# Optimization experiments

Measured on AMD Instinct MI355X. Metric: run time of the kernel, lower is better.

Reference implementation:

```python
import jax, jax.numpy as jnp
import numpy as np

ALPHA = 0.2  # leaky_relu negative slope
NEG = -1e20


def gat_conv(x, edges, W, a, b):
    # x: [B,N,F], W: [F,O], a: [2O,1], b: [O]
    h = jnp.einsum('bnf,fo->bno', x, W)
    O = W.shape[1]
    # cat([h[src], h[tgt]]) @ a  ==  h[src]@a[:O] + h[tgt]@a[O:]
    s1 = h @ a[:O, 0]   # [B,N]
    s2 = h @ a[O:, 0]   # [B,N]
    src, tgt = edges[0], edges[1]
    e = jax.nn.leaky_relu(s1[:, src] + s2[:, tgt], ALPHA)  # [B,E]
    B, N, _ = h.shape
    # dense NxN scatter-assign, as in the original module
    att = jnp.full((B, N, N), NEG, dtype=h.dtype).at[:, src, tgt].set(e)
    att = jax.nn.softmax(att, axis=-1)
    return jnp.einsum('bnm,bmo->bno', att, h) + b


def setup_inputs() -> dict:
    key = jax.random.key(0)
    ks = jax.random.split(key, 8)
    B, N, E = 2, 2048, 32768
    Fin, nhid, nhead, Fout = 256, 8, 8, 64
    x = jax.random.normal(ks[0], (B, N, Fin), dtype=jnp.float32)
    edges = jax.random.randint(ks[1], (2, E), 0, N)
    # xavier-like init (gain 1.414)
    W_h = jax.random.normal(ks[2], (nhead, Fin, nhid), dtype=jnp.float32) * (1.414 / np.sqrt(Fin))
    a_h = jax.random.normal(ks[3], (nhead, 2 * nhid, 1), dtype=jnp.float32) * 0.3
    b_h = jnp.zeros((nhead, nhid), dtype=jnp.float32)
    W_o = jax.random.normal(ks[4], (nhid * nhead, Fout), dtype=jnp.float32) * (1.414 / np.sqrt(nhid * nhead))
    a_o = jax.random.normal(ks[5], (2 * Fout, 1), dtype=jnp.float32) * 0.1
    b_o = jnp.zeros((Fout,), dtype=jnp.float32)
    return {'x': x, 'edges': edges, 'W_h': W_h, 'a_h': a_h, 'b_h': b_h,
            'W_o': W_o, 'a_o': a_o, 'b_o': b_o}


def reference(x, edges, W_h, a_h, b_h, W_o, a_o, b_o):
    B, N, _ = x.shape
    # nhead parallel GATConv heads, concatenated along feature dim
    heads = jax.vmap(lambda W, a, b: gat_conv(x, edges, W, a, b))(W_h, a_h, b_h)  # [H,B,N,nhid]
    x1 = jax.nn.elu(jnp.moveaxis(heads, 0, 2).reshape(B, N, -1))  # [B,N,H*nhid]
    out = gat_conv(x1, edges, W_o, a_o, b_o)  # single out head (mean of 1)
    return jax.nn.log_softmax(out, axis=1)  # softmax over the node dim, per original
```

## Files before the change

kernel.cpp:

```cpp
#include <hip/hip_runtime.h>

#define BB   2
#define NN   2048
#define FIN  256
#define HH   8
#define NHID 8
#define C1   64
#define FOUT 64
#define MAXD 192
#define FASTD 64
#define GB1  512

__global__ __launch_bounds__(256)
void k_front(const float* __restrict__ x, const float* __restrict__ Wh,
             const float* __restrict__ ah, const int* __restrict__ edges, int E,
             float* __restrict__ h1, float* __restrict__ s1h, float* __restrict__ s2h,
             int* __restrict__ cnt, int* __restrict__ csr)
{
    __shared__ float xs[8][FIN];
    int tid = threadIdx.x;

    if (blockIdx.x >= GB1) {
        int e = (blockIdx.x - GB1) * 256 + tid;
        if (e < E) {
            int s = edges[e], t = edges[E + e];
            int pos = atomicAdd(&cnt[s], 1);
            if (pos < MAXD) csr[s * MAXD + pos] = t;
        }
        return;
    }

    int base = blockIdx.x * 8;
    const float4* xv = (const float4*)(x + (size_t)base * FIN);
    float4* xsv = (float4*)&xs[0][0];
    xsv[tid] = xv[tid];
    xsv[tid + 256] = xv[tid + 256];
    __syncthreads();

    int wave = tid >> 6, lane = tid & 63;
    int head = lane >> 3, k = lane & 7;
    const float* Wp = Wh + head * FIN * NHID + k;
    int n0 = wave * 2;
    const float4* xr0 = (const float4*)xs[n0 + 0];
    const float4* xr1 = (const float4*)xs[n0 + 1];
    float a0 = 0.f, a1 = 0.f;
#pragma unroll 8
    for (int ff = 0; ff < FIN / 4; ++ff) {
        float4 v0 = xr0[ff], v1 = xr1[ff];
        float w0 = Wp[(4 * ff + 0) * NHID];
        float w1 = Wp[(4 * ff + 1) * NHID];
        float w2 = Wp[(4 * ff + 2) * NHID];
        float w3 = Wp[(4 * ff + 3) * NHID];
        a0 += w0 * v0.x; a0 += w1 * v0.y; a0 += w2 * v0.z; a0 += w3 * v0.w;
        a1 += w0 * v1.x; a1 += w1 * v1.y; a1 += w2 * v1.z; a1 += w3 * v1.w;
    }
    size_t hb = (size_t)(base + n0) * C1 + lane;
    h1[hb] = a0; h1[hb + C1] = a1;

    float c1 = ah[head * 16 + k], c2 = ah[head * 16 + 8 + k];
    float p0 = a0 * c1, p1 = a1 * c1;
    float q0 = a0 * c2, q1 = a1 * c2;
    for (int o = 1; o < 8; o <<= 1) {
        p0 += __shfl_xor(p0, o); p1 += __shfl_xor(p1, o);
        q0 += __shfl_xor(q0, o); q1 += __shfl_xor(q1, o);
    }
    if (k == 0) {
        float ps[2] = {p0, p1}, qs[2] = {q0, q1};
#pragma unroll
        for (int j = 0; j < 2; ++j) {
            int bn = base + n0 + j;
            s1h[(size_t)bn * HH + head] = ps[j];
            s2h[(size_t)bn * HH + head] = qs[j];
        }
    }
}

__global__ __launch_bounds__(256)
void k_att1g2(const float* __restrict__ h1, const float* __restrict__ s1h,
              const float* __restrict__ s2h, const float* __restrict__ bh,
              const int* __restrict__ cnt, int* __restrict__ csr,
              const float* __restrict__ Wo, const float* __restrict__ ao,
              float* __restrict__ h2, float* __restrict__ s1o, float* __restrict__ s2o)
{
    __shared__ int tg4[4][MAXD];
    __shared__ float es4[4][FASTD][HH];
    __shared__ float xs4[4][C1];
    int tid = threadIdx.x, w = tid >> 6, lane = tid & 63;
    int* tg = tg4[w];
    float* xs = xs4[w];
    int bn = blockIdx.x * 4 + w;
    int b = bn >> 11, n = bn & (NN - 1);
    int head = lane >> 3;

    int d = cnt[n]; if (d > MAXD) d = MAXD;
    for (int l = lane; l < d; l += 64) tg[l] = csr[n * MAXD + l];
    for (int l = lane; l < d; l += 64) {
        int t = tg[l], f = 0;
        for (int j = 0; j < l; ++j) f |= (tg[j] == t);
        if (f) tg[l] = -1;
    }
    for (int l = lane; l < d; l += 64) csr[n * MAXD + l] = tg[l];

    const float* hp = h1 + (size_t)b * NN * C1 + lane;
    float out;
    if (d == 0) {
        float acc = 0.f;
        for (int j = 0; j < NN; ++j) acc += hp[(size_t)j * C1];
        out = acc * (1.0f / NN);
    } else if (d <= FASTD) {
        const float* s2b = s2h + (size_t)b * NN * HH;
        for (int idx = lane; idx < d * HH; idx += 64) {
            int l = idx >> 3, hh = idx & 7;
            int t = tg[l];
            es4[w][l][hh] = s2b[(size_t)(t < 0 ? 0 : t) * HH + hh];
        }
        float s1 = s1h[(size_t)bn * HH + head];
        float m = -3.4e38f;
        for (int p = 0; p < d; ++p) {
            float ee = s1 + es4[w][p][head];
            ee = ee > 0.f ? ee : 0.2f * ee;
            m = fmaxf(m, tg[p] < 0 ? -3.4e38f : ee);
        }
        float den = 0.f, acc = 0.f;
        int p = 0;
        for (; p + 4 <= d; p += 4) {
            int t0 = tg[p], t1 = tg[p + 1], t2 = tg[p + 2], t3 = tg[p + 3];
            float v0 = hp[(size_t)(t0 < 0 ? 0 : t0) * C1];
            float v1 = hp[(size_t)(t1 < 0 ? 0 : t1) * C1];
            float v2 = hp[(size_t)(t2 < 0 ? 0 : t2) * C1];
            float v3 = hp[(size_t)(t3 < 0 ? 0 : t3) * C1];
            float e0 = s1 + es4[w][p + 0][head]; e0 = e0 > 0.f ? e0 : 0.2f * e0;
            float e1 = s1 + es4[w][p + 1][head]; e1 = e1 > 0.f ? e1 : 0.2f * e1;
            float e2 = s1 + es4[w][p + 2][head]; e2 = e2 > 0.f ? e2 : 0.2f * e2;
            float e3 = s1 + es4[w][p + 3][head]; e3 = e3 > 0.f ? e3 : 0.2f * e3;
            float w0 = t0 < 0 ? 0.f : expf(e0 - m);
            float w1 = t1 < 0 ? 0.f : expf(e1 - m);
            float w2 = t2 < 0 ? 0.f : expf(e2 - m);
            float w3 = t3 < 0 ? 0.f : expf(e3 - m);
            den += w0; acc += w0 * v0;
            den += w1; acc += w1 * v1;
            den += w2; acc += w2 * v2;
            den += w3; acc += w3 * v3;
        }
        for (; p < d; ++p) {
            int t = tg[p];
            float v = hp[(size_t)(t < 0 ? 0 : t) * C1];
            float ee = s1 + es4[w][p][head];
            ee = ee > 0.f ? ee : 0.2f * ee;
            float wt = t < 0 ? 0.f : expf(ee - m);
            den += wt; acc += wt * v;
        }
        out = acc / den;
    } else {
        float s1 = s1h[(size_t)bn * HH + head];
        const float* s2b = s2h + (size_t)b * NN * HH;
        float m = -3.4e38f;
        for (int p = 0; p < d; ++p) {
            int t = tg[p]; if (t < 0) continue;
            float ee = s1 + s2b[(size_t)t * HH + head];
            ee = ee > 0.f ? ee : 0.2f * ee;
            m = fmaxf(m, ee);
        }
        float den = 0.f, acc = 0.f;
        for (int p = 0; p < d; ++p) {
            int t = tg[p]; if (t < 0) continue;
            float ee = s1 + s2b[(size_t)t * HH + head];
            ee = ee > 0.f ? ee : 0.2f * ee;
            float wt = expf(ee - m);
            den += wt;
            acc += wt * hp[(size_t)t * C1];
        }
        out = acc / den;
    }
    out += bh[lane];
    xs[lane] = out > 0.f ? out : (expf(out) - 1.f);

    float acc2 = 0.f;
#pragma unroll 16
    for (int f = 0; f < C1; ++f) acc2 += xs[f] * Wo[f * FOUT + lane];
    h2[(size_t)bn * FOUT + lane] = acc2;
    float p = acc2 * ao[lane];
    float q = acc2 * ao[FOUT + lane];
    for (int o = 1; o < 64; o <<= 1) { p += __shfl_xor(p, o); q += __shfl_xor(q, o); }
    if (lane == 0) { s1o[bn] = p; s2o[bn] = q; }
}

__global__ __launch_bounds__(256)
void k_att2(const float* __restrict__ h2, const float* __restrict__ s1o,
            const float* __restrict__ s2o, const float* __restrict__ bo,
            const int* __restrict__ cnt, const int* __restrict__ csr,
            float* __restrict__ out2T)
{
    __shared__ int tg4[4][MAXD];
    __shared__ float es4[4][FASTD];
    int tid = threadIdx.x, w = tid >> 6, lane = tid & 63;
    int* tg = tg4[w];
    int bn = blockIdx.x * 4 + w;
    int b = bn >> 11, n = bn & (NN - 1);

    int d = cnt[n]; if (d > MAXD) d = MAXD;
    for (int l = lane; l < d; l += 64) tg[l] = csr[n * MAXD + l];

    const float* hp = h2 + (size_t)b * NN * FOUT + lane;
    const float* s2p = s2o + b * NN;
    float out;
    if (d == 0) {
        float acc = 0.f;
        for (int j = 0; j < NN; ++j) acc += hp[(size_t)j * FOUT];
        out = acc * (1.0f / NN);
    } else if (d <= FASTD) {
        for (int l = lane; l < d; l += 64) {
            int t = tg[l];
            es4[w][l] = s2p[t < 0 ? 0 : t];
        }
        float s1 = s1o[bn];
        float m = -3.4e38f;
        for (int p = 0; p < d; ++p) {
            float ee = s1 + es4[w][p];
            ee = ee > 0.f ? ee : 0.2f * ee;
            m = fmaxf(m, tg[p] < 0 ? -3.4e38f : ee);
        }
        float den = 0.f, acc = 0.f;
        int p = 0;
        for (; p + 4 <= d; p += 4) {
            int t0 = tg[p], t1 = tg[p + 1], t2 = tg[p + 2], t3 = tg[p + 3];
            float v0 = hp[(size_t)(t0 < 0 ? 0 : t0) * FOUT];
            float v1 = hp[(size_t)(t1 < 0 ? 0 : t1) * FOUT];
            float v2 = hp[(size_t)(t2 < 0 ? 0 : t2) * FOUT];
            float v3 = hp[(size_t)(t3 < 0 ? 0 : t3) * FOUT];
            float e0 = s1 + es4[w][p + 0]; e0 = e0 > 0.f ? e0 : 0.2f * e0;
            float e1 = s1 + es4[w][p + 1]; e1 = e1 > 0.f ? e1 : 0.2f * e1;
            float e2 = s1 + es4[w][p + 2]; e2 = e2 > 0.f ? e2 : 0.2f * e2;
            float e3 = s1 + es4[w][p + 3]; e3 = e3 > 0.f ? e3 : 0.2f * e3;
            float w0 = t0 < 0 ? 0.f : expf(e0 - m);
            float w1 = t1 < 0 ? 0.f : expf(e1 - m);
            float w2 = t2 < 0 ? 0.f : expf(e2 - m);
            float w3 = t3 < 0 ? 0.f : expf(e3 - m);
            den += w0; acc += w0 * v0;
            den += w1; acc += w1 * v1;
            den += w2; acc += w2 * v2;
            den += w3; acc += w3 * v3;
        }
        for (; p < d; ++p) {
            int t = tg[p];
            float v = hp[(size_t)(t < 0 ? 0 : t) * FOUT];
            float ee = s1 + es4[w][p];
            ee = ee > 0.f ? ee : 0.2f * ee;
            float wt = t < 0 ? 0.f : expf(ee - m);
            den += wt; acc += wt * v;
        }
        out = acc / den;
    } else {
        float s1 = s1o[bn];
        float m = -3.4e38f;
        for (int p = 0; p < d; ++p) {
            int t = tg[p]; if (t < 0) continue;
            float ee = s1 + s2p[t];
            ee = ee > 0.f ? ee : 0.2f * ee;
            m = fmaxf(m, ee);
        }
        float den = 0.f, acc = 0.f;
        for (int p = 0; p < d; ++p) {
            int t = tg[p]; if (t < 0) continue;
            float ee = s1 + s2p[t];
            ee = ee > 0.f ? ee : 0.2f * ee;
            float wt = expf(ee - m);
            den += wt;
            acc += wt * hp[(size_t)t * FOUT];
        }
        out = acc / den;
    }
    out2T[(size_t)(b * FOUT + lane) * NN + n] = out + bo[lane];
}

__global__ __launch_bounds__(256)
void k_lsef(const float* __restrict__ out2T, float* __restrict__ out)
{
    int row = blockIdx.x;
    int b = row >> 6, o = row & 63;
    int tid = threadIdx.x;
    const float* p = out2T + (size_t)row * NN;
    float v[8];
    float m = -3.4e38f;
#pragma unroll
    for (int j = 0; j < 8; ++j) {
        v[j] = p[tid + 256 * j];
        m = fmaxf(m, v[j]);
    }
    for (int off = 1; off < 64; off <<= 1) m = fmaxf(m, __shfl_xor(m, off));
    __shared__ float sm[4], ss[4];
    if ((tid & 63) == 0) sm[tid >> 6] = m;
    __syncthreads();
    float M = fmaxf(fmaxf(sm[0], sm[1]), fmaxf(sm[2], sm[3]));
    float sum = 0.f;
#pragma unroll
    for (int j = 0; j < 8; ++j) sum += expf(v[j] - M);
    for (int off = 1; off < 64; off <<= 1) sum += __shfl_xor(sum, off);
    if ((tid & 63) == 0) ss[tid >> 6] = sum;
    __syncthreads();
    float lse = M + logf(ss[0] + ss[1] + ss[2] + ss[3]);
    float* op = out + (size_t)b * NN * FOUT + o;
#pragma unroll
    for (int j = 0; j < 8; ++j) op[(size_t)(tid + 256 * j) * FOUT] = v[j] - lse;
}

extern "C" void kernel_launch(void* const* d_in, const int* in_sizes, int n_in,
                              void* d_out, int out_size, void* d_ws, size_t ws_size,
                              hipStream_t stream)
{
    (void)n_in; (void)out_size; (void)ws_size;
    const float* x     = (const float*)d_in[0];
    const int*   edges = (const int*)d_in[1];
    const float* Wh    = (const float*)d_in[2];
    const float* ah    = (const float*)d_in[3];
    const float* bh    = (const float*)d_in[4];
    const float* Wo    = (const float*)d_in[5];
    const float* ao    = (const float*)d_in[6];
    const float* bo    = (const float*)d_in[7];
    int E = in_sizes[1] / 2;

    char* w = (char*)d_ws;
    float* h1    = (float*)w; w += (size_t)BB * NN * C1 * 4;
    float* s1h   = (float*)w; w += (size_t)BB * NN * HH * 4;
    float* s2h   = (float*)w; w += (size_t)BB * NN * HH * 4;
    float* h2    = (float*)w; w += (size_t)BB * NN * FOUT * 4;
    float* s1o   = (float*)w; w += (size_t)BB * NN * 4;
    float* s2o   = (float*)w; w += (size_t)BB * NN * 4;
    float* out2T = (float*)w; w += (size_t)BB * FOUT * NN * 4;
    int*   cnt   = (int*)w;   w += (size_t)NN * 4;
    int*   csr   = (int*)w;   w += (size_t)NN * MAXD * 4;

    hipMemsetAsync(cnt, 0, (size_t)NN * 4, stream);

    int scatter_blocks = (E + 255) / 256;
    k_front <<<GB1 + scatter_blocks, 256, 0, stream>>>(x, Wh, ah, edges, E,
                                                       h1, s1h, s2h, cnt, csr);
    k_att1g2<<<BB * NN / 4, 256, 0, stream>>>(h1, s1h, s2h, bh, cnt, csr,
                                              Wo, ao, h2, s1o, s2o);
    k_att2  <<<BB * NN / 4, 256, 0, stream>>>(h2, s1o, s2o, bo, cnt, csr, out2T);
    k_lsef  <<<BB * FOUT, 256, 0, stream>>>(out2T, (float*)d_out);
}
```

Before: 110.7 us.

## Fuse all GAT stages into one cooperative kernel with grid syncs

After: 357.0 us. +222.6%, slower.

```diff
diff --git a/kernel.cpp b/kernel.cpp
--- a/kernel.cpp
+++ b/kernel.cpp
@@ -1,307 +1,323 @@
 #include <hip/hip_runtime.h>
-
-#define BB   2
-#define NN   2048
-#define FIN  256
-#define HH   8
-#define NHID 8
-#define C1   64
-#define FOUT 64
-#define MAXD 192
+#include <hip/hip_cooperative_groups.h>
+
+namespace cg = cooperative_groups;
+
+#define BB    2
+#define NN    2048
+#define FIN   256
+#define HH    8
+#define NHID  8
+#define C1    64
+#define FOUT  64
+#define MAXD  192
 #define FASTD 64
-#define GB1  512
-
-__global__ __launch_bounds__(256)
-void k_front(const float* __restrict__ x, const float* __restrict__ Wh,
-             const float* __restrict__ ah, const int* __restrict__ edges, int E,
-             float* __restrict__ h1, float* __restrict__ s1h, float* __restrict__ s2h,
-             int* __restrict__ cnt, int* __restrict__ csr)
+#define NB    512
+
+__global__ __launch_bounds__(256, 2)
+void k_gat(const float* __restrict__ x, const float* __restrict__ Wh,
+           const float* __restrict__ ah, const float* __restrict__ bh,
+           const float* __restrict__ Wo, const float* __restrict__ ao,
+           const float* __restrict__ bo, const int* __restrict__ edges, int E,
+           float* __restrict__ h1, float* __restrict__ s1h, float* __restrict__ s2h,
+           int* __restrict__ cnt, int* __restrict__ csr,
+           float* __restrict__ h2, float* __restrict__ s1o, float* __restrict__ s2o,
+           float* __restrict__ pm, float* __restrict__ ps, float* __restrict__ lse,
+           float* __restrict__ out)
 {
-    __shared__ float xs[8][FIN];
-    int tid = threadIdx.x;
-
-    if (blockIdx.x >= GB1) {
-        int e = (blockIdx.x - GB1) * 256 + tid;
-        if (e < E) {
+    cg::grid_group grid = cg::this_grid();
+
+    __shared__ union SMem {
+        float xs1[8][FIN];
+        struct { int tg[4][MAXD]; float es[4][FASTD][HH]; float xsg[4][C1]; } p2;
+        struct { int tg[4][MAXD]; float es[4][FASTD]; float vals[8][C1]; } p3;
+    } sm;
+
+    int tid = threadIdx.x, w = tid >> 6, lane = tid & 63;
+    int bb = blockIdx.x >> 8;
+
+    {
+        int base = blockIdx.x * 8;
+        const float4* xv = (const float4*)(x + (size_t)base * FIN);
+        float4* xsv = (float4*)&sm.xs1[0][0];
+        xsv[tid] = xv[tid];
+        xsv[tid + 256] = xv[tid + 256];
+
+        int epb = (E + NB - 1) / NB;
+        int e0 = blockIdx.x * epb;
+        int e1 = e0 + epb; if (e1 > E) e1 = E;
+        for (int e = e0 + tid; e < e1; e += 256) {
             int s = edges[e], t = edges[E + e];
             int pos = atomicAdd(&cnt[s], 1);
             if (pos < MAXD) csr[s * MAXD + pos] = t;
         }
-        return;
-    }
-
-    int base = blockIdx.x * 8;
-    const float4* xv = (const float4*)(x + (size_t)base * FIN);
-    float4* xsv = (float4*)&xs[0][0];
-    xsv[tid] = xv[tid];
-    xsv[tid + 256] = xv[tid + 256];
-    __syncthreads();
-
-    int wave = tid >> 6, lane = tid & 63;
-    int head = lane >> 3, k = lane & 7;
-    const float* Wp = Wh + head * FIN * NHID + k;
-    int n0 = wave * 2;
-    const float4* xr0 = (const float4*)xs[n0 + 0];
-    const float4* xr1 = (const float4*)xs[n0 + 1];
-    float a0 = 0.f, a1 = 0.f;
+        __syncthreads();
+
+        int head = lane >> 3, k = lane & 7;
+        const float* Wp = Wh + head * FIN * NHID + k;
+        int n0 = w * 2;
+        const float4* xr0 = (const float4*)sm.xs1[n0 + 0];
+        const float4* xr1 = (const float4*)sm.xs1[n0 + 1];
+        float a0 = 0.f, a1 = 0.f;
 #pragma unroll 8
-    for (int ff = 0; ff < FIN / 4; ++ff) {
-        float4 v0 = xr0[ff], v1 = xr1[ff];
-        float w0 = Wp[(4 * ff + 0) * NHID];
-        float w1 = Wp[(4 * ff + 1) * NHID];
-        float w2 = Wp[(4 * ff + 2) * NHID];
-        float w3 = Wp[(4 * ff + 3) * NHID];
-        a0 += w0 * v0.x; a0 += w1 * v0.y; a0 += w2 * v0.z; a0 += w3 * v0.w;
-        a1 += w0 * v1.x; a1 += w1 * v1.y; a1 += w2 * v1.z; a1 += w3 * v1.w;
-    }
-    size_t hb = (size_t)(base + n0) * C1 + lane;
-    h1[hb] = a0; h1[hb + C1] = a1;
-
-    float c1 = ah[head * 16 + k], c2 = ah[head * 16 + 8 + k];
-    float p0 = a0 * c1, p1 = a1 * c1;
-    float q0 = a0 * c2, q1 = a1 * c2;
-    for (int o = 1; o < 8; o <<= 1) {
-        p0 += __shfl_xor(p0, o); p1 += __shfl_xor(p1, o);
-        q0 += __shfl_xor(q0, o); q1 += __shfl_xor(q1, o);
-    }
-    if (k == 0) {
-        float ps[2] = {p0, p1}, qs[2] = {q0, q1};
+        for (int ff = 0; ff < FIN / 4; ++ff) {
+            float4 v0 = xr0[ff], v1 = xr1[ff];
+            float w0 = Wp[(4 * ff + 0) * NHID];
+            float w1 = Wp[(4 * ff + 1) * NHID];
+            float w2 = Wp[(4 * ff + 2) * NHID];
+            float w3 = Wp[(4 * ff + 3) * NHID];
+            a0 += w0 * v0.x; a0 += w1 * v0.y; a0 += w2 * v0.z; a0 += w3 * v0.w;
+            a1 += w0 * v1.x; a1 += w1 * v1.y; a1 += w2 * v1.z; a1 += w3 * v1.w;
+        }
+        size_t hb = (size_t)(base + n0) * C1 + lane;
+        h1[hb] = a0; h1[hb + C1] = a1;
+
+        float c1 = ah[head * 16 + k], c2 = ah[head * 16 + 8 + k];
+        float p0 = a0 * c1, p1 = a1 * c1;
+        float q0 = a0 * c2, q1 = a1 * c2;
+        for (int o = 1; o < 8; o <<= 1) {
+            p0 += __shfl_xor(p0, o); p1 += __shfl_xor(p1, o);
+            q0 += __shfl_xor(q0, o); q1 += __shfl_xor(q1, o);
+        }
+        if (k == 0) {
+            size_t bn0 = (size_t)(base + n0);
+            s1h[bn0 * HH + head] = p0;       s2h[bn0 * HH + head] = q0;
+            s1h[(bn0 + 1) * HH + head] = p1; s2h[(bn0 + 1) * HH + head] = q1;
+        }
+    }
+    grid.sync();
+
+    {
+        int* tg = sm.p2.tg[w];
+        float* xs = sm.p2.xsg[w];
+        int head = lane >> 3;
+#pragma unroll 2
+        for (int j = 0; j < 2; ++j) {
+            int bn = blockIdx.x * 8 + w * 2 + j;
+            int b = bn >> 11, n = bn & (NN - 1);
+
+            int d = cnt[n]; if (d > MAXD) d = MAXD;
+            for (int l = lane; l < d; l += 64) tg[l] = csr[n * MAXD + l];
+            for (int l = lane; l < d; l += 64) {
+                int t = tg[l], f = 0;
+                for (int jj = 0; jj < l; ++jj) f |= (tg[jj] == t);
+                if (f) tg[l] = -1;
+            }
+            if (b == 0)
+                for (int l = lane; l < d; l += 64) csr[n * MAXD + l] = tg[l];
+
+            const float* hp = h1 + (size_t)b * NN * C1 + lane;
+            float outv;
+            if (d == 0) {
+                float acc = 0.f;
+                for (int jj = 0; jj < NN; ++jj) acc += hp[(size_t)jj * C1];
+                outv = acc * (1.0f / NN);
+            } else if (d <= FASTD) {
+                const float* s2b = s2h + (size_t)b * NN * HH;
+                for (int idx = lane; idx < d * HH; idx += 64) {
+                    int l = idx >> 3, hh = idx & 7;
+                    int t = tg[l];
+                    sm.p2.es[w][l][hh] = s2b[(size_t)(t < 0 ? 0 : t) * HH + hh];
+                }
+                float s1 = s1h[(size_t)bn * HH + head];
+                float m = -3.4e38f;
+                for (int p = 0; p < d; ++p) {
+                    float ee = s1 + sm.p2.es[w][p][head];
+                    ee = ee > 0.f ? ee : 0.2f * ee;
+                    m = fmaxf(m, tg[p] < 0 ? -3.4e38f : ee);
+                }
+                float den = 0.f, acc = 0.f;
+                int p = 0;
+                for (; p + 4 <= d; p += 4) {
+                    int t0 = tg[p], t1 = tg[p + 1], t2 = tg[p + 2], t3 = tg[p + 3];
+                    float v0 = hp[(size_t)(t0 < 0 ? 0 : t0) * C1];
+                    float v1 = hp[(size_t)(t1 < 0 ? 0 : t1) * C1];
+                    float v2 = hp[(size_t)(t2 < 0 ? 0 : t2) * C1];
+                    float v3 = hp[(size_t)(t3 < 0 ? 0 : t3) * C1];
+                    float e0 = s1 + sm.p2.es[w][p + 0][head]; e0 = e0 > 0.f ? e0 : 0.2f * e0;
+                    float e1 = s1 + sm.p2.es[w][p + 1][head]; e1 = e1 > 0.f ? e1 : 0.2f * e1;
+                    float e2 = s1 + sm.p2.es[w][p + 2][head]; e2 = e2 > 0.f ? e2 : 0.2f * e2;
+                    float e3 = s1 + sm.p2.es[w][p + 3][head]; e3 = e3 > 0.f ? e3 : 0.2f * e3;
+                    float w0 = t0 < 0 ? 0.f : expf(e0 - m);
+                    float w1 = t1 < 0 ? 0.f : expf(e1 - m);
+                    float w2 = t2 < 0 ? 0.f : expf(e2 - m);
+                    float w3 = t3 < 0 ? 0.f : expf(e3 - m);
+                    den += w0; acc += w0 * v0;
+                    den += w1; acc += w1 * v1;
+                    den += w2; acc += w2 * v2;
+                    den += w3; acc += w3 * v3;
+                }
+                for (; p < d; ++p) {
+                    int t = tg[p];
+                    float v = hp[(size_t)(t < 0 ? 0 : t) * C1];
+                    float ee = s1 + sm.p2.es[w][p][head];
+                    ee = ee > 0.f ? ee : 0.2f * ee;
+                    float wt = t < 0 ? 0.f : expf(ee - m);
+                    den += wt; acc += wt * v;
+                }
+                outv = acc / den;
+            } else {
+                float s1 = s1h[(size_t)bn * HH + head];
+                const float* s2b = s2h + (size_t)b * NN * HH;
+                float m = -3.4e38f;
+                for (int p = 0; p < d; ++p) {
+                    int t = tg[p]; if (t < 0) continue;
+                    float ee = s1 + s2b[(size_t)t * HH + head];
+                    ee = ee > 0.f ? ee : 0.2f * ee;
+                    m = fmaxf(m, ee);
+                }
+                float den = 0.f, acc = 0.f;
+                for (int p = 0; p < d; ++p) {
+                    int t = tg[p]; if (t < 0) continue;
+                    float ee = s1 + s2b[(size_t)t * HH + head];
+                    ee = ee > 0.f ? ee : 0.2f * ee;
+                    float wt = expf(ee - m);
+                    den += wt;
+                    acc += wt * hp[(size_t)t * C1];
+                }
+                outv = acc / den;
+            }
+            outv += bh[lane];
+            xs[lane] = outv > 0.f ? outv : (expf(outv) - 1.f);
+
+            float acc2 = 0.f;
+#pragma unroll 16
+            for (int f = 0; f < C1; ++f) acc2 += xs[f] * Wo[f * FOUT + lane];
+            h2[(size_t)bn * FOUT + lane] = acc2;
+            float p = acc2 * ao[lane];
+            float q = acc2 * ao[FOUT + lane];
+            for (int o = 1; o < 64; o <<= 1) { p += __shfl_xor(p, o); q += __shfl_xor(q, o); }
+            if (lane == 0) { s1o[bn] = p; s2o[bn] = q; }
+        }
+    }
+    grid.sync();
+
+    float v01[2];
+    {
+        int* tg = sm.p3.tg[w];
+#pragma unroll 2
+        for (int j = 0; j < 2; ++j) {
+            int bn = blockIdx.x * 8 + w * 2 + j;
+            int b = bn >> 11, n = bn & (NN - 1);
+
+            int d = cnt[n]; if (d > MAXD) d = MAXD;
+            for (int l = lane; l < d; l += 64) tg[l] = csr[n * MAXD + l];
+
+            const float* hp = h2 + (size_t)b * NN * FOUT + lane;
+            const float* s2p = s2o + b * NN;
+            float outv;
+            if (d == 0) {
+                float acc = 0.f;
+                for (int jj = 0; jj < NN; ++jj) acc += hp[(size_t)jj * FOUT];
+                outv = acc * (1.0f / NN);
+            } else if (d <= FASTD) {
+                for (int l = lane; l < d; l += 64) {
+                    int t = tg[l];
+                    sm.p3.es[w][l] = s2p[t < 0 ? 0 : t];
+                }
+                float s1 = s1o[bn];
+                float m = -3.4e38f;
+                for (int p = 0; p < d; ++p) {
+                    float ee = s1 + sm.p3.es[w][p];
+                    ee = ee > 0.f ? ee : 0.2f * ee;
+                    m = fmaxf(m, tg[p] < 0 ? -3.4e38f : ee);
+                }
+                float den = 0.f, acc = 0.f;
+                int p = 0;
+                for (; p + 4 <= d; p += 4) {
+                    int t0 = tg[p], t1 = tg[p + 1], t2 = tg[p + 2], t3 = tg[p + 3];
+                    float v0 = hp[(size_t)(t0 < 0 ? 0 : t0) * FOUT];
+                    float v1 = hp[(size_t)(t1 < 0 ? 0 : t1) * FOUT];
+                    float v2 = hp[(size_t)(t2 < 0 ? 0 : t2) * FOUT];
+                    float v3 = hp[(size_t)(t3 < 0 ? 0 : t3) * FOUT];
+                    float e0 = s1 + sm.p3.es[w][p + 0]; e0 = e0 > 0.f ? e0 : 0.2f * e0;
+                    float e1 = s1 + sm.p3.es[w][p + 1]; e1 = e1 > 0.f ? e1 : 0.2f * e1;
+                    float e2 = s1 + sm.p3.es[w][p + 2]; e2 = e2 > 0.f ? e2 : 0.2f * e2;
+                    float e3 = s1 + sm.p3.es[w][p + 3]; e3 = e3 > 0.f ? e3 : 0.2f * e3;
+                    float w0 = t0 < 0 ? 0.f : expf(e0 - m);
+                    float w1 = t1 < 0 ? 0.f : expf(e1 - m);
+                    float w2 = t2 < 0 ? 0.f : expf(e2 - m);
+                    float w3 = t3 < 0 ? 0.f : expf(e3 - m);
+                    den += w0; acc += w0 * v0;
+                    den += w1; acc += w1 * v1;
+                    den += w2; acc += w2 * v2;
+                    den += w3; acc += w3 * v3;
+                }
+                for (; p < d; ++p) {
+                    int t = tg[p];
+                    float v = hp[(size_t)(t < 0 ? 0 : t) * FOUT];
+                    float ee = s1 + sm.p3.es[w][p];
+                    ee = ee > 0.f ? ee : 0.2f * ee;
+                    float wt = t < 0 ? 0.f : expf(ee - m);
+                    den += wt; acc += wt * v;
+                }
+                outv = acc / den;
+            } else {
+                float s1 = s1o[bn];
+                float m = -3.4e38f;
+                for (int p = 0; p < d; ++p) {
+                    int t = tg[p]; if (t < 0) continue;
+                    float ee = s1 + s2p[t];
+                    ee = ee > 0.f ? ee : 0.2f * ee;
+                    m = fmaxf(m, ee);
+                }
+                float den = 0.f, acc = 0.f;
+                for (int p = 0; p < d; ++p) {
+                    int t = tg[p]; if (t < 0) continue;
+                    float ee = s1 + s2p[t];
+                    ee = ee > 0.f ? ee : 0.2f * ee;
+                    float wt = expf(ee - m);
+                    den += wt;
+                    acc += wt * hp[(size_t)t * FOUT];
+                }
+                outv = acc / den;
+            }
+            v01[j] = outv + bo[lane];
+        }
+
+        sm.p3.vals[w * 2 + 0][lane] = v01[0];
+        sm.p3.vals[w * 2 + 1][lane] = v01[1];
+        __syncthreads();
+        if (w == 0) {
+            float m = -3.4e38f;
 #pragma unroll
-        for (int j = 0; j < 2; ++j) {
-            int bn = base + n0 + j;
-            s1h[(size_t)bn * HH + head] = ps[j];
-            s2h[(size_t)bn * HH + head] = qs[j];
-        }
-    }
-}
-
-__global__ __launch_bounds__(256)
-void k_att1g2(const float* __restrict__ h1, const float* __restrict__ s1h,
-              const float* __restrict__ s2h, const float* __restrict__ bh,
-              const int* __restrict__ cnt, int* __restrict__ csr,
-              const float* __restrict__ Wo, const float* __restrict__ ao,
-              float* __restrict__ h2, float* __restrict__ s1o, float* __restrict__ s2o)
-{
-    __shared__ int tg4[4][MAXD];
-    __shared__ float es4[4][FASTD][HH];
-    __shared__ float xs4[4][C1];
-    int tid = threadIdx.x, w = tid >> 6, lane = tid & 63;
-    int* tg = tg4[w];
-    float* xs = xs4[w];
-    int bn = blockIdx.x * 4 + w;
-    int b = bn >> 11, n = bn & (NN - 1);
-    int head = lane >> 3;
-
-    int d = cnt[n]; if (d > MAXD) d = MAXD;
-    for (int l = lane; l < d; l += 64) tg[l] = csr[n * MAXD + l];
-    for (int l = lane; l < d; l += 64) {
-        int t = tg[l], f = 0;
-        for (int j = 0; j < l; ++j) f |= (tg[j] == t);
-        if (f) tg[l] = -1;
-    }
-    for (int l = lane; l < d; l += 64) csr[n * MAXD + l] = tg[l];
-
-    const float* hp = h1 + (size_t)b * NN * C1 + lane;
-    float out;
-    if (d == 0) {
-        float acc = 0.f;
-        for (int j = 0; j < NN; ++j) acc += hp[(size_t)j * C1];
-        out = acc * (1.0f / NN);
-    } else if (d <= FASTD) {
-        const float* s2b = s2h + (size_t)b * NN * HH;
-        for (int idx = lane; idx < d * HH; idx += 64) {
-            int l = idx >> 3, hh = idx & 7;
-            int t = tg[l];
-            es4[w][l][hh] = s2b[(size_t)(t < 0 ? 0 : t) * HH + hh];
-        }
-        float s1 = s1h[(size_t)bn * HH + head];
-        float m = -3.4e38f;
-        for (int p = 0; p < d; ++p) {
-            float ee = s1 + es4[w][p][head];
-            ee = ee > 0.f ? ee : 0.2f * ee;
-            m = fmaxf(m, tg[p] < 0 ? -3.4e38f : ee);
-        }
-        float den = 0.f, acc = 0.f;
-        int p = 0;
-        for (; p + 4 <= d; p += 4) {
-            int t0 = tg[p], t1 = tg[p + 1], t2 = tg[p + 2], t3 = tg[p + 3];
-            float v0 = hp[(size_t)(t0 < 0 ? 0 : t0) * C1];
-            float v1 = hp[(size_t)(t1 < 0 ? 0 : t1) * C1];
-            float v2 = hp[(size_t)(t2 < 0 ? 0 : t2) * C1];
-            float v3 = hp[(size_t)(t3 < 0 ? 0 : t3) * C1];
-            float e0 = s1 + es4[w][p + 0][head]; e0 = e0 > 0.f ? e0 : 0.2f * e0;
-            float e1 = s1 + es4[w][p + 1][head]; e1 = e1 > 0.f ? e1 : 0.2f * e1;
-            float e2 = s1 + es4[w][p + 2][head]; e2 = e2 > 0.f ? e2 : 0.2f * e2;
-            float e3 = s1 + es4[w][p + 3][head]; e3 = e3 > 0.f ? e3 : 0.2f * e3;
-            float w0 = t0 < 0 ? 0.f : expf(e0 - m);
-            float w1 = t1 < 0 ? 0.f : expf(e1 - m);
-            float w2 = t2 < 0 ? 0.f : expf(e2 - m);
-            float w3 = t3 < 0 ? 0.f : expf(e3 - m);
-            den += w0; acc += w0 * v0;
-            den += w1; acc += w1 * v1;
-            den += w2; acc += w2 * v2;
-            den += w3; acc += w3 * v3;
-        }
-        for (; p < d; ++p) {
-            int t = tg[p];
-            float v = hp[(size_t)(t < 0 ? 0 : t) * C1];
-            float ee = s1 + es4[w][p][head];
-            ee = ee > 0.f ? ee : 0.2f * ee;
-            float wt = t < 0 ? 0.f : expf(ee - m);
-            den += wt; acc += wt * v;
-        }
-        out = acc / den;
-    } else {
-        float s1 = s1h[(size_t)bn * HH + head];
-        const float* s2b = s2h + (size_t)b * NN * HH;
-        float m = -3.4e38f;
-        for (int p = 0; p < d; ++p) {
-            int t = tg[p]; if (t < 0) continue;
-            float ee = s1 + s2b[(size_t)t * HH + head];
-            ee = ee > 0.f ? ee : 0.2f * ee;
-            m = fmaxf(m, ee);
-        }
-        float den = 0.f, acc = 0.f;
-        for (int p = 0; p < d; ++p) {
-            int t = tg[p]; if (t < 0) continue;
-            float ee = s1 + s2b[(size_t)t * HH + head];
-            ee = ee > 0.f ? ee : 0.2f * ee;
-            float wt = expf(ee - m);
-            den += wt;
-            acc += wt * hp[(size_t)t * C1];
-        }
-        out = acc / den;
-    }
-    out += bh[lane];
-    xs[lane] = out > 0.f ? out : (expf(out) - 1.f);
-
-    float acc2 = 0.f;
-#pragma unroll 16
-    for (int f = 0; f < C1; ++f) acc2 += xs[f] * Wo[f * FOUT + lane];
-    h2[(size_t)bn * FOUT + lane] = acc2;
-    float p = acc2 * ao[lane];
-    float q = acc2 * ao[FOUT + lane];
-    for (int o = 1; o < 64; o <<= 1) { p += __shfl_xor(p, o); q += __shfl_xor(q, o); }
-    if (lane == 0) { s1o[bn] = p; s2o[bn] = q; }
-}
-
-__global__ __launch_bounds__(256)
-void k_att2(const float* __restrict__ h2, const float* __restrict__ s1o,
-            const float* __restrict__ s2o, const float* __restrict__ bo,
-            const int* __restrict__ cnt, const int* __restrict__ csr,
-            float* __restrict__ out2T)
-{
-    __shared__ int tg4[4][MAXD];
-    __shared__ float es4[4][FASTD];
-    int tid = threadIdx.x, w = tid >> 6, lane = tid & 63;
-    int* tg = tg4[w];
-    int bn = blockIdx.x * 4 + w;
-    int b = bn >> 11, n = bn & (NN - 1);
-
-    int d = cnt[n]; if (d > MAXD) d = MAXD;
-    for (int l = lane; l < d; l += 64) tg[l] = csr[n * MAXD + l];
-
-    const float* hp = h2 + (size_t)b * NN * FOUT + lane;
-    const float* s2p = s2o + b * NN;
-    float out;
-    if (d == 0) {
-        float acc = 0.f;
-        for (int j = 0; j < NN; ++j) acc += hp[(size_t)j * FOUT];
-        out = acc * (1.0f / NN);
-    } else if (d <= FASTD) {
-        for (int l = lane; l < d; l += 64) {
-            int t = tg[l];
-            es4[w][l] = s2p[t < 0 ? 0 : t];
-        }
-        float s1 = s1o[bn];
-        float m = -3.4e38f;
-        for (int p = 0; p < d; ++p) {
-            float ee = s1 + es4[w][p];
-            ee = ee > 0.f ? ee : 0.2f * ee;
-            m = fmaxf(m, tg[p] < 0 ? -3.4e38f : ee);
-        }
-        float den = 0.f, acc = 0.f;
-        int p = 0;
-        for (; p + 4 <= d; p += 4) {
-            int t0 = tg[p], t1 = tg[p + 1], t2 = tg[p + 2], t3 = tg[p + 3];
-            float v0 = hp[(size_t)(t0 < 0 ? 0 : t0) * FOUT];
-            float v1 = hp[(size_t)(t1 < 0 ? 0 : t1) * FOUT];
-            float v2 = hp[(size_t)(t2 < 0 ? 0 : t2) * FOUT];
-            float v3 = hp[(size_t)(t3 < 0 ? 0 : t3) * FOUT];
-            float e0 = s1 + es4[w][p + 0]; e0 = e0 > 0.f ? e0 : 0.2f * e0;
-            float e1 = s1 + es4[w][p + 1]; e1 = e1 > 0.f ? e1 : 0.2f * e1;
-            float e2 = s1 + es4[w][p + 2]; e2 = e2 > 0.f ? e2 : 0.2f * e2;
-            float e3 = s1 + es4[w][p + 3]; e3 = e3 > 0.f ? e3 : 0.2f * e3;
-            float w0 = t0 < 0 ? 0.f : expf(e0 - m);
-            float w1 = t1 < 0 ? 0.f : expf(e1 - m);
-            float w2 = t2 < 0 ? 0.f : expf(e2 - m);
-            float w3 = t3 < 0 ? 0.f : expf(e3 - m);
-            den += w0; acc += w0 * v0;
-            den += w1; acc += w1 * v1;
-            den += w2; acc += w2 * v2;
-            den += w3; acc += w3 * v3;
-        }
-        for (; p < d; ++p) {
-            int t = tg[p];
-            float v = hp[(size_t)(t < 0 ? 0 : t) * FOUT];
-            float ee = s1 + es4[w][p];
-            ee = ee > 0.f ? ee : 0.2f * ee;
-            float wt = t < 0 ? 0.f : expf(ee - m);
-            den += wt; acc += wt * v;
-        }
-        out = acc / den;
-    } else {
-        float s1 = s1o[bn];
-        float m = -3.4e38f;
-        for (int p = 0; p < d; ++p) {
-            int t = tg[p]; if (t < 0) continue;
-            float ee = s1 + s2p[t];
-            ee = ee > 0.f ? ee : 0.2f * ee;
-            m = fmaxf(m, ee);
-        }
-        float den = 0.f, acc = 0.f;
-        for (int p = 0; p < d; ++p) {
-            int t = tg[p]; if (t < 0) continue;
-            float ee = s1 + s2p[t];
-            ee = ee > 0.f ? ee : 0.2f * ee;
-            float wt = expf(ee - m);
-            den += wt;
-            acc += wt * hp[(size_t)t * FOUT];
-        }
-        out = acc / den;
-    }
-    out2T[(size_t)(b * FOUT + lane) * NN + n] = out + bo[lane];
-}
-
-__global__ __launch_bounds__(256)
-void k_lsef(const float* __restrict__ out2T, float* __restrict__ out)
-{
-    int row = blockIdx.x;
-    int b = row >> 6, o = row & 63;
-    int tid = threadIdx.x;
-    const float* p = out2T + (size_t)row * NN;
-    float v[8];
-    float m = -3.4e38f;
+            for (int i = 0; i < 8; ++i) m = fmaxf(m, sm.p3.vals[i][lane]);
+            float s = 0.f;
 #pragma unroll
-    for (int j = 0; j < 8; ++j) {
-        v[j] = p[tid + 256 * j];
-        m = fmaxf(m, v[j]);
-    }
-    for (int off = 1; off < 64; off <<= 1) m = fmaxf(m, __shfl_xor(m, off));
-    __shared__ float sm[4], ss[4];
-    if ((tid & 63) == 0) sm[tid >> 6] = m;
-    __syncthreads();
-    float M = fmaxf(fmaxf(sm[0], sm[1]), fmaxf(sm[2], sm[3]));
-    float sum = 0.f;
+            for (int i = 0; i < 8; ++i) s += expf(sm.p3.vals[i][lane] - m);
+            int c = blockIdx.x & 255;
+            size_t r = (size_t)(bb * FOUT + lane);
+            pm[r * 256 + c] = m;
+            ps[r * 256 + c] = s;
+        }
+    }
+    grid.sync();
+
+    if (blockIdx.x < BB * FOUT && w == 0) {
+        size_t r = blockIdx.x;
+        float mv[4], sv[4];
+        float M = -3.4e38f;
 #pragma unroll
-    for (int j = 0; j < 8; ++j) sum += expf(v[j] - M);
-    for (int off = 1; off < 64; off <<= 1) sum += __shfl_xor(sum, off);
-    if ((tid & 63) == 0) ss[tid >> 6] = sum;
-    __syncthreads();
-    float lse = M + logf(ss[0] + ss[1] + ss[2] + ss[3]);
-    float* op = out + (size_t)b * NN * FOUT + o;
+        for (int i = 0; i < 4; ++i) {
+            mv[i] = pm[r * 256 + lane + 64 * i];
+            sv[i] = ps[r * 256 + lane + 64 * i];
+            M = fmaxf(M, mv[i]);
+        }
+        for (int o = 1; o < 64; o <<= 1) M = fmaxf(M, __shfl_xor(M, o));
+        float S = 0.f;
 #pragma unroll
-    for (int j = 0; j < 8; ++j) op[(size_t)(tid + 256 * j) * FOUT] = v[j] - lse;
+        for (int i = 0; i < 4; ++i) S += sv[i] * expf(mv[i] - M);
+        for (int o = 1; o < 64; o <<= 1) S += __shfl_xor(S, o);
+        if (lane == 0) lse[r] = M + logf(S);
+    }
+    grid.sync();
+
+    {
+        float l0 = lse[bb * FOUT + lane];
+        size_t bn0 = (size_t)blockIdx.x * 8 + w * 2;
+        out[bn0 * FOUT + lane] = v01[0] - l0;
+        out[(bn0 + 1) * FOUT + lane] = v01[1] - l0;
+    }
 }
 
 extern "C" void kernel_launch(void* const* d_in, const int* in_sizes, int n_in,
@@ -318,25 +334,28 @@
     const float* ao    = (const float*)d_in[6];
     const float* bo    = (const float*)d_in[7];
     int E = in_sizes[1] / 2;
+    float* outp = (float*)d_out;
 
     char* w = (char*)d_ws;
-    float* h1    = (float*)w; w += (size_t)BB * NN * C1 * 4;
-    float* s1h   = (float*)w; w += (size_t)BB * NN * HH * 4;
-    float* s2h   = (float*)w; w += (size_t)BB * NN * HH * 4;
-    float* h2    = (float*)w; w += (size_t)BB * NN * FOUT * 4;
-    float* s1o   = (float*)w; w += (size_t)BB * NN * 4;
-    float* s2o   = (float*)w; w += (size_t)BB * NN * 4;
-    float* out2T = (float*)w; w += (size_t)BB * FOUT * NN * 4;
-    int*   cnt   = (int*)w;   w += (size_t)NN * 4;
-    int*   csr   = (int*)w;   w += (size_t)NN * MAXD * 4;
+    float* h1  = (float*)w; w += (size_t)BB * NN * C1 * 4;
+    float* s1h = (float*)w; w += (size_t)BB * NN * HH * 4;
+    float* s2h = (float*)w; w += (size_t)BB * NN * HH * 4;
+    float* h2  = (float*)w; w += (size_t)BB * NN * FOUT * 4;
+    float* s1o = (float*)w; w += (size_t)BB * NN * 4;
+    float* s2o = (float*)w; w += (size_t)BB * NN * 4;
+    float* pm  = (float*)w; w += (size_t)BB * FOUT * 256 * 4;
+    float* ps  = (float*)w; w += (size_t)BB * FOUT * 256 * 4;
+    float* lse = (float*)w; w += 4096;
+    int*   cnt = (int*)w;   w += (size_t)NN * 4;
+    int*   csr = (int*)w;   w += (size_t)NN * MAXD * 4;
 
     hipMemsetAsync(cnt, 0, (size_t)NN * 4, stream);
 
-    int scatter_blocks = (E + 255) / 256;
-    k_front <<<GB1 + scatter_blocks, 256, 0, stream>>>(x, Wh, ah, edges, E,
-                                                       h1, s1h, s2h, cnt, csr);
-    k_att1g2<<<BB * NN / 4, 256, 0, stream>>>(h1, s1h, s2h, bh, cnt, csr,
-                                              Wo, ao, h2, s1o, s2o);
-    k_att2  <<<BB * NN / 4, 256, 0, stream>>>(h2, s1o, s2o, bo, cnt, csr, out2T);
-    k_lsef  <<<BB * FOUT, 256, 0, stream>>>(out2T, (float*)d_out);
+    void* args[] = {(void*)&x, (void*)&Wh, (void*)&ah, (void*)&bh,
+                    (void*)&Wo, (void*)&ao, (void*)&bo, (void*)&edges, (void*)&E,
+                    (void*)&h1, (void*)&s1h, (void*)&s2h, (void*)&cnt, (void*)&csr,
+                    (void*)&h2, (void*)&s1o, (void*)&s2o,
+                    (void*)&pm, (void*)&ps, (void*)&lse, (void*)&outp};
+    hipLaunchCooperativeKernel(reinterpret_cast<const void*>(k_gat),
+                               dim3(NB), dim3(256), args, 0u, stream);
 }
```

## Fuse partial log-softmax stats into att2 and split final normalization

Applied to the files above, without the earlier changes.

After: 111.8 us. About the same (+1.0%).

```diff
diff --git a/kernel.cpp b/kernel.cpp
--- a/kernel.cpp
+++ b/kernel.cpp
@@ -1,15 +1,16 @@
 #include <hip/hip_runtime.h>
 
-#define BB   2
-#define NN   2048
-#define FIN  256
-#define HH   8
-#define NHID 8
-#define C1   64
-#define FOUT 64
-#define MAXD 192
+#define BB    2
+#define NN    2048
+#define FIN   256
+#define HH    8
+#define NHID  8
+#define C1    64
+#define FOUT  64
+#define MAXD  192
 #define FASTD 64
-#define GB1  512
+#define GB1   512
+#define CHUNK 512
 
 __global__ __launch_bounds__(256)
 void k_front(const float* __restrict__ x, const float* __restrict__ Wh,
@@ -65,12 +66,12 @@
         q0 += __shfl_xor(q0, o); q1 += __shfl_xor(q1, o);
     }
     if (k == 0) {
-        float ps[2] = {p0, p1}, qs[2] = {q0, q1};
+        float psv[2] = {p0, p1}, qsv[2] = {q0, q1};
 #pragma unroll
         for (int j = 0; j < 2; ++j) {
             int bn = base + n0 + j;
-            s1h[(size_t)bn * HH + head] = ps[j];
-            s2h[(size_t)bn * HH + head] = qs[j];
+            s1h[(size_t)bn * HH + head] = psv[j];
+            s2h[(size_t)bn * HH + head] = qsv[j];
         }
     }
 }
@@ -186,13 +187,14 @@
 }
 
 __global__ __launch_bounds__(256)
-void k_att2(const float* __restrict__ h2, const float* __restrict__ s1o,
-            const float* __restrict__ s2o, const float* __restrict__ bo,
-            const int* __restrict__ cnt, const int* __restrict__ csr,
-            float* __restrict__ out2T)
+void k_att2b(const float* __restrict__ h2, const float* __restrict__ s1o,
+             const float* __restrict__ s2o, const float* __restrict__ bo,
+             const int* __restrict__ cnt, const int* __restrict__ csr,
+             float* __restrict__ out2, float* __restrict__ pm, float* __restrict__ ps)
 {
     __shared__ int tg4[4][MAXD];
     __shared__ float es4[4][FASTD];
+    __shared__ float vals[4][C1];
     int tid = threadIdx.x, w = tid >> 6, lane = tid & 63;
     int* tg = tg4[w];
     int bn = blockIdx.x * 4 + w;
@@ -270,38 +272,67 @@
         }
         out = acc / den;
     }
-    out2T[(size_t)(b * FOUT + lane) * NN + n] = out + bo[lane];
-}
-
-__global__ __launch_bounds__(256)
-void k_lsef(const float* __restrict__ out2T, float* __restrict__ out)
-{
-    int row = blockIdx.x;
-    int b = row >> 6, o = row & 63;
-    int tid = threadIdx.x;
-    const float* p = out2T + (size_t)row * NN;
-    float v[8];
-    float m = -3.4e38f;
+    float v = out + bo[lane];
+    out2[(size_t)bn * FOUT + lane] = v;
+    vals[w][lane] = v;
+    __syncthreads();
+    if (w == 0) {
+        float m = -3.4e38f;
 #pragma unroll
-    for (int j = 0; j < 8; ++j) {
-        v[j] = p[tid + 256 * j];
-        m = fmaxf(m, v[j]);
-    }
-    for (int off = 1; off < 64; off <<= 1) m = fmaxf(m, __shfl_xor(m, off));
-    __shared__ float sm[4], ss[4];
-    if ((tid & 63) == 0) sm[tid >> 6] = m;
+        for (int i = 0; i < 4; ++i) m = fmaxf(m, vals[i][lane]);
+        float s = 0.f;
+#pragma unroll
+        for (int i = 0; i < 4; ++i) s += expf(vals[i][lane] - m);
+        int c = blockIdx.x & (CHUNK - 1);
+        int r = b * FOUT + lane;
+        pm[c * (BB * FOUT) + r] = m;
+        ps[c * (BB * FOUT) + r] = s;
+    }
+}
+
+__global__ __launch_bounds__(256)
+void k_merge(const float* __restrict__ pm, const float* __restrict__ ps,
+             float* __restrict__ lse)
+{
+    int r = blockIdx.x;
+    int tid = threadIdx.x, w = tid >> 6, lane = tid & 63;
+    float m = -3.4e38f, s = 0.f;
+    for (int c = tid; c < CHUNK; c += 256) {
+        float mm = pm[c * (BB * FOUT) + r], ss = ps[c * (BB * FOUT) + r];
+        float M = fmaxf(m, mm);
+        s = s * expf(m - M) + ss * expf(mm - M);
+        m = M;
+    }
+    for (int o = 1; o < 64; o <<= 1) {
+        float mm = __shfl_xor(m, o), ss = __shfl_xor(s, o);
+        float M = fmaxf(m, mm);
+        s = s * expf(m - M) + ss * expf(mm - M);
+        m = M;
+    }
+    __shared__ float smx[4], ssm[4];
+    if (lane == 0) { smx[w] = m; ssm[w] = s; }
     __syncthreads();
-    float M = fmaxf(fmaxf(sm[0], sm[1]), fmaxf(sm[2], sm[3]));
-    float sum = 0.f;
-#pragma unroll
-    for (int j = 0; j < 8; ++j) sum += expf(v[j] - M);
-    for (int off = 1; off < 64; off <<= 1) sum += __shfl_xor(sum, off);
-    if ((tid & 63) == 0) ss[tid >> 6] = sum;
-    __syncthreads();
-    float lse = M + logf(ss[0] + ss[1] + ss[2] + ss[3]);
-    float* op = out + (size_t)b * NN * FOUT + o;
-#pragma unroll
-    for (int j = 0; j < 8; ++j) op[(size_t)(tid + 256 * j) * FOUT] = v[j] - lse;
+    if (tid == 0) {
+        float M = fmaxf(fmaxf(smx[0], smx[1]), fmaxf(smx[2], smx[3]));
+        float S = ssm[0] * expf(smx[0] - M) + ssm[1] * expf(smx[1] - M)
+                + ssm[2] * expf(smx[2] - M) + ssm[3] * expf(smx[3] - M);
+        lse[r] = M + logf(S);
+    }
+}
+
+__global__ __launch_bounds__(256)
+void k_sub(const float* __restrict__ out2, const float* __restrict__ lse,
+           float* __restrict__ out)
+{
+    int idx = blockIdx.x * 256 + threadIdx.x;
+    float4 v = ((const float4*)out2)[idx];
+    int f0 = idx * 4;
+    int b = f0 >> 17;
+    int o = f0 & (FOUT - 1);
+    float4 l = *(const float4*)&lse[b * FOUT + o];
+    float4 rv;
+    rv.x = v.x - l.x; rv.y = v.y - l.y; rv.z = v.z - l.z; rv.w = v.w - l.w;
+    ((float4*)out)[idx] = rv;
 }
 
 extern "C" void kernel_launch(void* const* d_in, const int* in_sizes, int n_in,
@@ -320,15 +351,18 @@
     int E = in_sizes[1] / 2;
 
     char* w = (char*)d_ws;
-    float* h1    = (float*)w; w += (size_t)BB * NN * C1 * 4;
-    float* s1h   = (float*)w; w += (size_t)BB * NN * HH * 4;
-    float* s2h   = (float*)w; w += (size_t)BB * NN * HH * 4;
-    float* h2    = (float*)w; w += (size_t)BB * NN * FOUT * 4;
-    float* s1o   = (float*)w; w += (size_t)BB * NN * 4;
-    float* s2o   = (float*)w; w += (size_t)BB * NN * 4;
-    float* out2T = (float*)w; w += (size_t)BB * FOUT * NN * 4;
-    int*   cnt   = (int*)w;   w += (size_t)NN * 4;
-    int*   csr   = (int*)w;   w += (size_t)NN * MAXD * 4;
+    float* h1   = (float*)w; w += (size_t)BB * NN * C1 * 4;
+    float* s1h  = (float*)w; w += (size_t)BB * NN * HH * 4;
+    float* s2h  = (float*)w; w += (size_t)BB * NN * HH * 4;
+    float* h2   = (float*)w; w += (size_t)BB * NN * FOUT * 4;
+    float* s1o  = (float*)w; w += (size_t)BB * NN * 4;
+    float* s2o  = (float*)w; w += (size_t)BB * NN * 4;
+    float* out2 = (float*)w; w += (size_t)BB * NN * FOUT * 4;
+    float* pm   = (float*)w; w += (size_t)CHUNK * BB * FOUT * 4;
+    float* ps   = (float*)w; w += (size_t)CHUNK * BB * FOUT * 4;
+    float* lse  = (float*)w; w += 4096;
+    int*   cnt  = (int*)w;   w += (size_t)NN * 4;
+    int*   csr  = (int*)w;   w += (size_t)NN * MAXD * 4;
 
     hipMemsetAsync(cnt, 0, (size_t)NN * 4, stream);
 
@@ -337,6 +371,8 @@
                                                        h1, s1h, s2h, cnt, csr);
     k_att1g2<<<BB * NN / 4, 256, 0, stream>>>(h1, s1h, s2h, bh, cnt, csr,
                                               Wo, ao, h2, s1o, s2o);
-    k_att2  <<<BB * NN / 4, 256, 0, stream>>>(h2, s1o, s2o, bo, cnt, csr, out2T);
-    k_lsef  <<<BB * FOUT, 256, 0, stream>>>(out2T, (float*)d_out);
-}
+    k_att2b <<<BB * NN / 4, 256, 0, stream>>>(h2, s1o, s2o, bo, cnt, csr,
+                                              out2, pm, ps);
+    k_merge <<<BB * FOUT, 256, 0, stream>>>(pm, ps, lse);
+    k_sub   <<<BB * NN * FOUT / 4 / 256, 256, 0, stream>>>(out2, lse, (float*)d_out);
+}
```
